# Kernel tuning notes

Measured on AMD Instinct MI355X. Metric: run time of the kernel, lower is better.

Reference implementation:

```python
import jax, jax.numpy as jnp
import numpy as np

RANK, CHAN = 64, 128
B, N = 16, 4096

def setup_inputs() -> dict:
    key = jax.random.key(0)
    ks = jax.random.split(key, 12)
    s = lambda k, shp: jax.random.normal(k, shp, dtype=jnp.float32) * 0.05
    return {
        "z0": jax.random.normal(ks[0], (B, N, CHAN), dtype=jnp.float32),
        "z1": jax.random.normal(ks[1], (B, N, 3, CHAN), dtype=jnp.float32),
        "W0l": s(ks[2], (RANK, CHAN)), "b0l": s(ks[3], (RANK,)),
        "W0r": s(ks[4], (RANK, CHAN)), "b0r": s(ks[5], (RANK,)),
        "W1l": s(ks[6], (RANK, CHAN)),
        "W1r": s(ks[7], (RANK, CHAN)),
        "W0o": s(ks[8], (CHAN, 2 * RANK)), "b0o": s(ks[9], (CHAN,)),
        "W1o": s(ks[10], (CHAN, 3 * RANK)),
    }

def reference(z0, z1, W0l, b0l, W0r, b0r, W1l, W1r, W0o, b0o, W1o):
    # small projections chan -> rank
    z0_l = jnp.einsum("bnc,rc->bnr", z0, W0l) + b0l          # (B,N,R)
    z0_r = jnp.einsum("bnc,rc->bnr", z0, W0r) + b0r          # (B,N,R)
    z1_l = jnp.einsum("bnic,rc->bnir", z1, W1l)              # (B,N,3,R)
    z1_r = jnp.einsum("bnic,rc->bnir", z1, W1r)              # (B,N,3,R)

    # o0 paths: (0,0,0) scalar*scalar, (1,1,0) vector dot vector
    p00 = z0_l * z0_r                                        # (B,N,R)
    p110 = jnp.sum(z1_l * z1_r, axis=-2)                     # (B,N,R)
    z0_o = jnp.concatenate([p00, p110], axis=-1)             # (B,N,2R)

    # o1 paths: (0,1,1) scalar*vector, (1,0,1) vector*scalar, (1,1,1) cross
    q011 = z0_l[..., None, :] * z1_r                         # (B,N,3,R)
    q101 = z1_l * z0_r[..., None, :]                         # (B,N,3,R)
    q111 = jnp.cross(z1_l, z1_r, axis=-2)                    # (B,N,3,R)
    # ir_mul layout transposed to channels: (irrep_dim, num_irreps*rank)
    z1_o = jnp.concatenate([q011, q101, q111], axis=-1)      # (B,N,3,3R)

    out0 = jnp.einsum("bnk,ck->bnc", z0_o, W0o) + b0o        # (B,N,C)
    out1 = jnp.einsum("bnik,ck->bnic", z1_o, W1o)            # (B,N,3,C)
    return out0, out1
```

## Files before the change

kernel.cpp:

```cpp
#include <hip/hip_runtime.h>


typedef float  f32x4  __attribute__((ext_vector_type(4)));
typedef __bf16 bf16x8 __attribute__((ext_vector_type(8)));

#define LDS_BYTES 22528
#define P1_BASE   4096
#define P1_STRIDE 6144

#define FA_ID(mat,n,k) (((mat)*4+(n))*4+(k))
#define FB0_ID(n8,k)   (64 + (n8)*4 + (k))
#define FB1_ID(n8,k6)  (96 + (n8)*6 + (k6))
#define NFRAG 144
#define WS_NEED (NFRAG * 64 * 16)

__device__ __forceinline__ unsigned packbf(float lo, float hi) {
    unsigned a = (unsigned)__builtin_bit_cast(unsigned short, (__bf16)lo);
    unsigned b = (unsigned)__builtin_bit_cast(unsigned short, (__bf16)hi);
    return a | (b << 16);
}
__device__ __forceinline__ void st_bf(void* p, float v) {
    *(unsigned short*)p = __builtin_bit_cast(unsigned short, (__bf16)v);
}
__device__ __forceinline__ bf16x8 cvtW(const float* p) {
    float4 a = *(const float4*)p;
    float4 b = *(const float4*)(p + 4);
    bf16x8 r;
    r[0] = (__bf16)a.x; r[1] = (__bf16)a.y; r[2] = (__bf16)a.z; r[3] = (__bf16)a.w;
    r[4] = (__bf16)b.x; r[5] = (__bf16)b.y; r[6] = (__bf16)b.z; r[7] = (__bf16)b.w;
    return r;
}
__device__ __forceinline__ f32x4 mm(bf16x8 a, bf16x8 b, f32x4 c) {
    return __builtin_amdgcn_mfma_f32_16x16x32_bf16(a, b, c, 0, 0, 0);
}

__device__ __forceinline__ int map_b0(int kk) { return (kk & 1) ? 64 + (kk >> 1) : (kk >> 1); }
__device__ __forceinline__ int map_b1(int kk) { return kk >= 128 ? kk : ((kk & 1) ? 64 + (kk >> 1) : (kk >> 1)); }

__device__ __forceinline__ bf16x8 gatherB0(const float* W0o, int n8, int k, int lr, int lg) {
    bf16x8 r; const int c = n8 * 16 + lr;
    #pragma unroll
    for (int e = 0; e < 8; ++e) r[e] = (__bf16)W0o[c * 128 + map_b0(k * 32 + lg * 8 + e)];
    return r;
}
__device__ __forceinline__ bf16x8 gatherB1(const float* W1o, int n8, int k6, int lr, int lg) {
    bf16x8 r; const int c = n8 * 16 + lr;
    #pragma unroll
    for (int e = 0; e < 8; ++e) r[e] = (__bf16)W1o[c * 192 + map_b1(k6 * 32 + lg * 8 + e)];
    return r;
}

__global__ void etp_setup(const float* __restrict__ W0l, const float* __restrict__ W0r,
                          const float* __restrict__ W1l, const float* __restrict__ W1r,
                          const float* __restrict__ W0o, const float* __restrict__ W1o,
                          bf16x8* __restrict__ wsf)
{
    const int gid = blockIdx.x * 256 + threadIdx.x;
    if (gid >= NFRAG * 64) return;
    const int fid = gid >> 6, l = gid & 63, lr = l & 15, lg = l >> 4;
    bf16x8 r;
    if (fid < 64) {
        const int mat = fid >> 4, n = (fid >> 2) & 3, k = fid & 3;
        const float* Wm = (mat == 0) ? W0l : (mat == 1) ? W0r : (mat == 2) ? W1l : W1r;
        r = cvtW(Wm + (n * 16 + lr) * 128 + k * 32 + lg * 8);
    } else if (fid < 96) {
        const int f = fid - 64;
        r = gatherB0(W0o, f >> 2, f & 3, lr, lg);
    } else {
        const int f = fid - 96;
        r = gatherB1(W1o, f / 6, f % 6, lr, lg);
    }
    wsf[fid * 64 + l] = r;
}

template <bool WS>
__global__ __launch_bounds__(64, 2)
void etp_main(const float* __restrict__ z0, const float* __restrict__ z1,
              const float* __restrict__ W0l, const float* __restrict__ b0l,
              const float* __restrict__ W0r, const float* __restrict__ b0r,
              const float* __restrict__ W1l, const float* __restrict__ W1r,
              const float* __restrict__ W0o, const float* __restrict__ b0o,
              const float* __restrict__ W1o,
              const bf16x8* __restrict__ wsf,
              float* __restrict__ out0, float* __restrict__ out1)
{
    __shared__ __align__(16) unsigned char smem[LDS_BYTES];
    const int l  = threadIdx.x;
    const int lr = l & 15;
    const int lg = l >> 4;
    const int m0 = blockIdx.x * 16;

    bf16x8 za0[4], za1[3][4];
    #pragma unroll
    for (int k = 0; k < 4; ++k)
        za0[k] = cvtW(z0 + (size_t)(m0 + lr) * 128 + k * 32 + lg * 8);
    #pragma unroll
    for (int i = 0; i < 3; ++i)
        #pragma unroll
        for (int k = 0; k < 4; ++k)
            za1[i][k] = cvtW(z1 + ((size_t)(m0 + lr) * 3 + i) * 128 + k * 32 + lg * 8);

    f32x4 zero = {0.f, 0.f, 0.f, 0.f};
    f32x4 aL0[4], aR0[4], aL1[3][4], aR1[3][4];
    #pragma unroll
    for (int n = 0; n < 4; ++n) {
        aL0[n] = zero; aR0[n] = zero;
        #pragma unroll
        for (int i = 0; i < 3; ++i) { aL1[i][n] = zero; aR1[i][n] = zero; }
    }
    #pragma unroll
    for (int n = 0; n < 4; ++n) {
        #pragma unroll
        for (int k = 0; k < 4; ++k) {
            bf16x8 w0 = WS ? wsf[FA_ID(0, n, k) * 64 + l]
                           : cvtW(W0l + (n * 16 + lr) * 128 + k * 32 + lg * 8);
            bf16x8 w1 = WS ? wsf[FA_ID(1, n, k) * 64 + l]
                           : cvtW(W0r + (n * 16 + lr) * 128 + k * 32 + lg * 8);
            bf16x8 w2 = WS ? wsf[FA_ID(2, n, k) * 64 + l]
                           : cvtW(W1l + (n * 16 + lr) * 128 + k * 32 + lg * 8);
            bf16x8 w3 = WS ? wsf[FA_ID(3, n, k) * 64 + l]
                           : cvtW(W1r + (n * 16 + lr) * 128 + k * 32 + lg * 8);
            aL0[n] = mm(za0[k], w0, aL0[n]);
            aR0[n] = mm(za0[k], w1, aR0[n]);
            #pragma unroll
            for (int i = 0; i < 3; ++i) {
                aL1[i][n] = mm(za1[i][k], w2, aL1[i][n]);
                aR1[i][n] = mm(za1[i][k], w3, aR1[i][n]);
            }
        }
    }
    #pragma unroll
    for (int n = 0; n < 4; ++n) {
        const float blv = b0l[n * 16 + lr], brv = b0r[n * 16 + lr];
        #pragma unroll
        for (int j = 0; j < 4; ++j) { aL0[n][j] += blv; aR0[n][j] += brv; }
    }

    #pragma unroll
    for (int n = 0; n < 4; ++n)
        #pragma unroll
        for (int j = 0; j < 4; ++j) {
            const int row = lg * 4 + j, sw = (row & 7) << 4;
            const float p00  = aL0[n][j] * aR0[n][j];
            const float p110 = aL1[0][n][j] * aR1[0][n][j]
                             + aL1[1][n][j] * aR1[1][n][j]
                             + aL1[2][n][j] * aR1[2][n][j];
            *(unsigned*)(smem + row * 256 + ((4 * (n * 16 + lr)) ^ sw)) = packbf(p00, p110);
        }
    #pragma unroll
    for (int i = 0; i < 3; ++i) {
        const int i1 = (i == 2) ? 0 : i + 1;
        const int i2 = (i == 0) ? 2 : i - 1;
        unsigned char* base = smem + P1_BASE + i * P1_STRIDE;
        #pragma unroll
        for (int n = 0; n < 4; ++n)
            #pragma unroll
            for (int j = 0; j < 4; ++j) {
                const int row = lg * 4 + j, sw = (row & 7) << 4;
                const float q011 = aL0[n][j] * aR1[i][n][j];
                const float q101 = aL1[i][n][j] * aR0[n][j];
                const float q111 = aL1[i1][n][j] * aR1[i2][n][j]
                                 - aL1[i2][n][j] * aR1[i1][n][j];
                *(unsigned*)(base + row * 384 + ((4 * (n * 16 + lr)) ^ sw)) = packbf(q011, q101);
                st_bf(base + row * 384 + ((256 + 2 * (n * 16 + lr)) ^ sw), q111);
            }
    }

    bf16x8 pa0[4], pa1[3][6];
    #pragma unroll
    for (int k = 0; k < 4; ++k)
        pa0[k] = *(const bf16x8*)(smem + lr * 256 + ((k * 64 + lg * 16) ^ ((lr & 7) << 4)));
    #pragma unroll
    for (int i = 0; i < 3; ++i)
        #pragma unroll
        for (int k6 = 0; k6 < 6; ++k6)
            pa1[i][k6] = *(const bf16x8*)(smem + P1_BASE + i * P1_STRIDE + lr * 384 +
                                          ((k6 * 64 + lg * 16) ^ ((lr & 7) << 4)));

    #pragma unroll
    for (int n8 = 0; n8 < 8; ++n8) {
        f32x4 o0 = zero, o1[3] = {zero, zero, zero};
        #pragma unroll
        for (int k = 0; k < 4; ++k) {
            bf16x8 b = WS ? wsf[FB0_ID(n8, k) * 64 + l] : gatherB0(W0o, n8, k, lr, lg);
            o0 = mm(pa0[k], b, o0);
        }
        #pragma unroll
        for (int k6 = 0; k6 < 6; ++k6) {
            bf16x8 b = WS ? wsf[FB1_ID(n8, k6) * 64 + l] : gatherB1(W1o, n8, k6, lr, lg);
            #pragma unroll
            for (int i = 0; i < 3; ++i) o1[i] = mm(pa1[i][k6], b, o1[i]);
        }
        const int c = n8 * 16 + lr;
        const float bo = b0o[c];
        #pragma unroll
        for (int j = 0; j < 4; ++j) {
            const size_t t = m0 + lg * 4 + j;
            out0[t * 128 + c] = o0[j] + bo;
            #pragma unroll
            for (int i = 0; i < 3; ++i)
                out1[(t * 3 + i) * 128 + c] = o1[i][j];
        }
    }
}

extern "C" void kernel_launch(void* const* d_in, const int* in_sizes, int n_in,
                              void* d_out, int out_size, void* d_ws, size_t ws_size,
                              hipStream_t stream)
{
    const float* z0  = (const float*)d_in[0];
    const float* z1  = (const float*)d_in[1];
    const float* W0l = (const float*)d_in[2];
    const float* b0l = (const float*)d_in[3];
    const float* W0r = (const float*)d_in[4];
    const float* b0r = (const float*)d_in[5];
    const float* W1l = (const float*)d_in[6];
    const float* W1r = (const float*)d_in[7];
    const float* W0o = (const float*)d_in[8];
    const float* b0o = (const float*)d_in[9];
    const float* W1o = (const float*)d_in[10];

    const int tokens = in_sizes[0] / 128;
    float* out0 = (float*)d_out;
    float* out1 = out0 + (size_t)tokens * 128;
    bf16x8* wsf = (bf16x8*)d_ws;

    if (ws_size >= (size_t)WS_NEED) {
        hipLaunchKernelGGL(etp_setup, dim3((NFRAG * 64 + 255) / 256), dim3(256), 0, stream,
                           W0l, W0r, W1l, W1r, W0o, W1o, wsf);
        hipLaunchKernelGGL((etp_main<true>), dim3(tokens / 16), dim3(64), 0, stream,
                           z0, z1, W0l, b0l, W0r, b0r, W1l, W1r, W0o, b0o, W1o,
                           wsf, out0, out1);
    } else {
        hipLaunchKernelGGL((etp_main<false>), dim3(tokens / 16), dim3(64), 0, stream,
                           z0, z1, W0l, b0l, W0r, b0r, W1l, W1r, W0o, b0o, W1o,
                           wsf, out0, out1);
    }
}
```

Before: 289.9 us.

## Swap MFMA operands to keep first-stage products in registers, shrink LDS

Transposes the first-stage MFMA so accumulators hold consecutive rank values per token, letting the bilinear products be packed directly into bf16 A fragments for the output GEMM. Only the cross-product term still goes through a small LDS buffer, reducing LDS from 22KB to 6KB and live accumulator registers. Launch bounds are raised to allow more waves per SIMD. Risks register spills under the tighter budget.

```diff
diff --git a/kernel.cpp b/kernel.cpp
--- a/kernel.cpp
+++ b/kernel.cpp
@@ -4,9 +4,7 @@
 typedef float  f32x4  __attribute__((ext_vector_type(4)));
 typedef __bf16 bf16x8 __attribute__((ext_vector_type(8)));
 
-#define LDS_BYTES 22528
-#define P1_BASE   4096
-#define P1_STRIDE 6144
+#define LDS_BYTES 6144
 
 #define FA_ID(mat,n,k) (((mat)*4+(n))*4+(k))
 #define FB0_ID(n8,k)   (64 + (n8)*4 + (k))
@@ -18,9 +16,6 @@
     unsigned a = (unsigned)__builtin_bit_cast(unsigned short, (__bf16)lo);
     unsigned b = (unsigned)__builtin_bit_cast(unsigned short, (__bf16)hi);
     return a | (b << 16);
-}
-__device__ __forceinline__ void st_bf(void* p, float v) {
-    *(unsigned short*)p = __builtin_bit_cast(unsigned short, (__bf16)v);
 }
 __device__ __forceinline__ bf16x8 cvtW(const float* p) {
     float4 a = *(const float4*)p;
@@ -32,6 +27,12 @@
 }
 __device__ __forceinline__ f32x4 mm(bf16x8 a, bf16x8 b, f32x4 c) {
     return __builtin_amdgcn_mfma_f32_16x16x32_bf16(a, b, c, 0, 0, 0);
+}
+__device__ __forceinline__ bf16x8 pack8(f32x4 a, f32x4 b) {
+    bf16x8 r;
+    #pragma unroll
+    for (int j = 0; j < 4; ++j) { r[2 * j] = (__bf16)a[j]; r[2 * j + 1] = (__bf16)b[j]; }
+    return r;
 }
 
 __device__ __forceinline__ int map_b0(int kk) { return (kk & 1) ? 64 + (kk >> 1) : (kk >> 1); }
@@ -74,7 +75,7 @@
 }
 
 template <bool WS>
-__global__ __launch_bounds__(64, 2)
+__global__ __launch_bounds__(64, 4)
 void etp_main(const float* __restrict__ z0, const float* __restrict__ z1,
               const float* __restrict__ W0l, const float* __restrict__ b0l,
               const float* __restrict__ W0r, const float* __restrict__ b0r,
@@ -90,92 +91,67 @@
     const int lg = l >> 4;
     const int m0 = blockIdx.x * 16;
 
-    bf16x8 za0[4], za1[3][4];
+    bf16x8 zb0[4], zb1[3][4];
     #pragma unroll
     for (int k = 0; k < 4; ++k)
-        za0[k] = cvtW(z0 + (size_t)(m0 + lr) * 128 + k * 32 + lg * 8);
+        zb0[k] = cvtW(z0 + (size_t)(m0 + lr) * 128 + k * 32 + lg * 8);
     #pragma unroll
     for (int i = 0; i < 3; ++i)
         #pragma unroll
         for (int k = 0; k < 4; ++k)
-            za1[i][k] = cvtW(z1 + ((size_t)(m0 + lr) * 3 + i) * 128 + k * 32 + lg * 8);
-
-    f32x4 zero = {0.f, 0.f, 0.f, 0.f};
-    f32x4 aL0[4], aR0[4], aL1[3][4], aR1[3][4];
-    #pragma unroll
-    for (int n = 0; n < 4; ++n) {
-        aL0[n] = zero; aR0[n] = zero;
-        #pragma unroll
-        for (int i = 0; i < 3; ++i) { aL1[i][n] = zero; aR1[i][n] = zero; }
-    }
-    #pragma unroll
-    for (int n = 0; n < 4; ++n) {
+            zb1[i][k] = cvtW(z1 + ((size_t)(m0 + lr) * 3 + i) * 128 + k * 32 + lg * 8);
+
+    const f32x4 zero = {0.f, 0.f, 0.f, 0.f};
+    bf16x8 pa0[4], pa1[3][4];
+    #pragma unroll
+    for (int mt = 0; mt < 4; ++mt) {
+        f32x4 L0 = zero, R0 = zero, L1[3] = {zero, zero, zero}, R1[3] = {zero, zero, zero};
         #pragma unroll
         for (int k = 0; k < 4; ++k) {
-            bf16x8 w0 = WS ? wsf[FA_ID(0, n, k) * 64 + l]
-                           : cvtW(W0l + (n * 16 + lr) * 128 + k * 32 + lg * 8);
-            bf16x8 w1 = WS ? wsf[FA_ID(1, n, k) * 64 + l]
-                           : cvtW(W0r + (n * 16 + lr) * 128 + k * 32 + lg * 8);
-            bf16x8 w2 = WS ? wsf[FA_ID(2, n, k) * 64 + l]
-                           : cvtW(W1l + (n * 16 + lr) * 128 + k * 32 + lg * 8);
-            bf16x8 w3 = WS ? wsf[FA_ID(3, n, k) * 64 + l]
-                           : cvtW(W1r + (n * 16 + lr) * 128 + k * 32 + lg * 8);
-            aL0[n] = mm(za0[k], w0, aL0[n]);
-            aR0[n] = mm(za0[k], w1, aR0[n]);
+            bf16x8 w0 = WS ? wsf[FA_ID(0, mt, k) * 64 + l]
+                           : cvtW(W0l + (mt * 16 + lr) * 128 + k * 32 + lg * 8);
+            bf16x8 w1 = WS ? wsf[FA_ID(1, mt, k) * 64 + l]
+                           : cvtW(W0r + (mt * 16 + lr) * 128 + k * 32 + lg * 8);
+            bf16x8 w2 = WS ? wsf[FA_ID(2, mt, k) * 64 + l]
+                           : cvtW(W1l + (mt * 16 + lr) * 128 + k * 32 + lg * 8);
+            bf16x8 w3 = WS ? wsf[FA_ID(3, mt, k) * 64 + l]
+                           : cvtW(W1r + (mt * 16 + lr) * 128 + k * 32 + lg * 8);
+            L0 = mm(w0, zb0[k], L0);
+            R0 = mm(w1, zb0[k], R0);
             #pragma unroll
             for (int i = 0; i < 3; ++i) {
-                aL1[i][n] = mm(za1[i][k], w2, aL1[i][n]);
-                aR1[i][n] = mm(za1[i][k], w3, aR1[i][n]);
+                L1[i] = mm(w2, zb1[i][k], L1[i]);
+                R1[i] = mm(w3, zb1[i][k], R1[i]);
             }
         }
-    }
-    #pragma unroll
-    for (int n = 0; n < 4; ++n) {
-        const float blv = b0l[n * 16 + lr], brv = b0r[n * 16 + lr];
-        #pragma unroll
-        for (int j = 0; j < 4; ++j) { aL0[n][j] += blv; aR0[n][j] += brv; }
-    }
-
-    #pragma unroll
-    for (int n = 0; n < 4; ++n)
-        #pragma unroll
-        for (int j = 0; j < 4; ++j) {
-            const int row = lg * 4 + j, sw = (row & 7) << 4;
-            const float p00  = aL0[n][j] * aR0[n][j];
-            const float p110 = aL1[0][n][j] * aR1[0][n][j]
-                             + aL1[1][n][j] * aR1[1][n][j]
-                             + aL1[2][n][j] * aR1[2][n][j];
-            *(unsigned*)(smem + row * 256 + ((4 * (n * 16 + lr)) ^ sw)) = packbf(p00, p110);
-        }
-    #pragma unroll
-    for (int i = 0; i < 3; ++i) {
-        const int i1 = (i == 2) ? 0 : i + 1;
-        const int i2 = (i == 0) ? 2 : i - 1;
-        unsigned char* base = smem + P1_BASE + i * P1_STRIDE;
-        #pragma unroll
-        for (int n = 0; n < 4; ++n)
-            #pragma unroll
-            for (int j = 0; j < 4; ++j) {
-                const int row = lg * 4 + j, sw = (row & 7) << 4;
-                const float q011 = aL0[n][j] * aR1[i][n][j];
-                const float q101 = aL1[i][n][j] * aR0[n][j];
-                const float q111 = aL1[i1][n][j] * aR1[i2][n][j]
-                                 - aL1[i2][n][j] * aR1[i1][n][j];
-                *(unsigned*)(base + row * 384 + ((4 * (n * 16 + lr)) ^ sw)) = packbf(q011, q101);
-                st_bf(base + row * 384 + ((256 + 2 * (n * 16 + lr)) ^ sw), q111);
-            }
-    }
-
-    bf16x8 pa0[4], pa1[3][6];
-    #pragma unroll
-    for (int k = 0; k < 4; ++k)
-        pa0[k] = *(const bf16x8*)(smem + lr * 256 + ((k * 64 + lg * 16) ^ ((lr & 7) << 4)));
+        L0 += *(const f32x4*)(b0l + mt * 16 + lg * 4);
+        R0 += *(const f32x4*)(b0r + mt * 16 + lg * 4);
+
+        const f32x4 p00  = L0 * R0;
+        const f32x4 p110 = L1[0] * R1[0] + L1[1] * R1[1] + L1[2] * R1[2];
+        pa0[mt] = pack8(p00, p110);
+        #pragma unroll
+        for (int i = 0; i < 3; ++i) {
+            const int i1 = (i == 2) ? 0 : i + 1;
+            const int i2 = (i == 0) ? 2 : i - 1;
+            const f32x4 q011 = L0 * R1[i];
+            const f32x4 q101 = L1[i] * R0;
+            pa1[i][mt] = pack8(q011, q101);
+            const f32x4 q111 = L1[i1] * R1[i2] - L1[i2] * R1[i1];
+            const int o = lr * 128 + mt * 32 + lg * 8;
+            *(uint2*)(smem + i * 2048 + (o ^ ((lr & 7) << 4))) =
+                make_uint2(packbf(q111[0], q111[1]), packbf(q111[2], q111[3]));
+        }
+    }
+
+    bf16x8 pq[3][2];
     #pragma unroll
     for (int i = 0; i < 3; ++i)
         #pragma unroll
-        for (int k6 = 0; k6 < 6; ++k6)
-            pa1[i][k6] = *(const bf16x8*)(smem + P1_BASE + i * P1_STRIDE + lr * 384 +
-                                          ((k6 * 64 + lg * 16) ^ ((lr & 7) << 4)));
+        for (int k2 = 0; k2 < 2; ++k2) {
+            const int o = lr * 128 + k2 * 64 + lg * 16;
+            pq[i][k2] = *(const bf16x8*)(smem + i * 2048 + (o ^ ((lr & 7) << 4)));
+        }
 
     #pragma unroll
     for (int n8 = 0; n8 < 8; ++n8) {
@@ -189,7 +165,8 @@
         for (int k6 = 0; k6 < 6; ++k6) {
             bf16x8 b = WS ? wsf[FB1_ID(n8, k6) * 64 + l] : gatherB1(W1o, n8, k6, lr, lg);
             #pragma unroll
-            for (int i = 0; i < 3; ++i) o1[i] = mm(pa1[i][k6], b, o1[i]);
+            for (int i = 0; i < 3; ++i)
+                o1[i] = mm(k6 < 4 ? pa1[i][k6] : pq[i][k6 - 4], b, o1[i]);
         }
         const int c = n8 * 16 + lr;
         const float bo = b0o[c];
```

New measurement: 377.2 us. +30.1%, slower.
